# Optimization experiments

Measured on AMD Instinct MI355X. Metric: run time of the kernel, lower is better.

## Reference

```python
import jax, jax.numpy as jnp
import numpy as np

D_MODEL = 768
N_HEADS = 12
D_HEAD = 64
WINDOW = 32
LOOK_BACK = 1
PAD_VALUE = 0
IGNORE = -1000000.0
BS = 2
SEQ = 1024  # multiple of WINDOW so autopad is a no-op


def setup_inputs() -> dict:
    key = jax.random.key(0)
    k0, k1, k2, k3, k4 = jax.random.split(key, 5)
    x = jax.random.normal(k0, (BS, SEQ, D_MODEL), dtype=jnp.float32)
    W_abcde = jax.random.normal(k1, (D_MODEL, 5 * N_HEADS * D_HEAD), dtype=jnp.float32) * (1.0 / np.sqrt(D_MODEL))
    b_abcde = jax.random.normal(k2, (5 * N_HEADS * D_HEAD,), dtype=jnp.float32) * 0.02
    W_O = jax.random.normal(k3, (N_HEADS * D_HEAD, D_MODEL), dtype=jnp.float32) * (1.0 / np.sqrt(N_HEADS * D_HEAD))
    b_O = jax.random.normal(k4, (D_MODEL,), dtype=jnp.float32) * 0.02
    return dict(x=x, W_abcde=W_abcde, b_abcde=b_abcde, W_O=W_O, b_O=b_O)


def _look_around(t, backward=LOOK_BACK, pad_value=0):
    # t: (B, n_windows, window, ...). Pad along the windows axis, then
    # concatenate [prev_window, current_window] along the within-window axis.
    nw = t.shape[1]
    pad = [(0, 0)] * t.ndim
    pad[1] = (backward, 0)
    tp = jnp.pad(t, pad, constant_values=pad_value)
    return jnp.concatenate([tp[:, i:i + nw] for i in range(backward + 1)], axis=2)


def reference(x, W_abcde, b_abcde, W_O, b_O):
    bs, ts, _ = x.shape
    nw = ts // WINDOW
    B = bs * N_HEADS

    abcde = x @ W_abcde + b_abcde                       # (bs, ts, 5*h*d)
    abcde = abcde.reshape(bs, ts, 5, N_HEADS, D_HEAD)
    abcde = jnp.transpose(abcde, (2, 0, 3, 1, 4))       # (5, bs, h, ts, d)
    abcde = abcde.reshape(5, B, nw, WINDOW, D_HEAD)     # windowed
    a, b, c, d, e = abcde[0], abcde[1], abcde[2], abcde[3], abcde[4]

    # position ids per window, and their look-around version (pad_value = cfg.pad_value)
    seq = jnp.arange(ts, dtype=jnp.int32).reshape(1, nw, WINDOW)      # (1, nw, w)
    bb_t = _look_around(seq, LOOK_BACK, PAD_VALUE)                    # (1, nw, 2w)
    qi = seq[..., :, None, None]    # query position  (n axis)
    kj = bb_t[..., None, :, None]   # a-token position (m axis)
    lk = bb_t[..., None, None, :]   # b-token position (l axis)
    # masked unless: t_b <= t_query AND t_a < t_b
    mask = (qi < lk) | (lk <= kj)   # (1, nw, w, 2w, 2w)

    la_a = _look_around(a)
    la_b = _look_around(b)
    la_d = _look_around(d)
    la_e = _look_around(e)

    # triple-interaction scores: (B, nw, w, 2w, 2w)
    attn = jnp.einsum('xnid,xnjd,xnkd->xnijk', c, la_a, la_b)
    # mask causal-invalid entries, and (as in original) exact zeros (padding dots)
    attn = jnp.where(mask | (attn == 0.0), IGNORE, attn)
    attn = attn / D_HEAD
    shp = attn.shape
    score = jax.nn.softmax(attn.reshape(shp[0], shp[1], shp[2], -1), axis=-1).reshape(shp)

    # dual value combine: D at the a-position (m), E at the b-position (l)
    z = jnp.einsum('xnijk,xnjd->xnid', score, la_d) \
        + jnp.einsum('xnijk,xnkd->xnid', score, la_e)

    z = z.reshape(bs, N_HEADS, nw, WINDOW, D_HEAD)
    z = jnp.transpose(z, (0, 2, 3, 1, 4)).reshape(bs, ts, N_HEADS * D_HEAD)
    return z @ W_O + b_O
```

## Files before the change

kernel.cpp:

```cpp
#include <hip/hip_runtime.h>
#include <math.h>
#include <stdint.h>

#define NH     12
#define DH     64
#define WIN    32
#define SEQL   1024
#define BSZ    2
#define NW     (SEQL / WIN)
#define DMODEL 768
#define NCOL   (5 * NH * DH)

typedef __attribute__((ext_vector_type(4))) float f32x4;
typedef __attribute__((ext_vector_type(8))) short bf16x8;
typedef unsigned short u16;

static __device__ __forceinline__ u16 f2bf(float f) {
  union { float f; unsigned u; } v; v.f = f;
  unsigned r = v.u + 0x7fffu + ((v.u >> 16) & 1u);
  return (u16)(r >> 16);
}
static __device__ __forceinline__ float bf2f(u16 u) {
  union { unsigned u; float f; } v; v.u = ((unsigned)u) << 16;
  return v.f;
}

typedef const __attribute__((address_space(1))) unsigned int* as1_cu32;
typedef __attribute__((address_space(3))) unsigned int* as3_u32;
static __device__ __forceinline__ void gload_lds16(const void* g, void* l) {
  __builtin_amdgcn_global_load_lds(
      reinterpret_cast<as1_cu32>(reinterpret_cast<uintptr_t>(g)),
      reinterpret_cast<as3_u32>(reinterpret_cast<uintptr_t>(l)), 16, 0, 0);
}

__global__ __launch_bounds__(256)
void cvt_bf16_kernel(const float* __restrict__ S, u16* __restrict__ D, int n4) {
  const int i = blockIdx.x * 256 + threadIdx.x;
  if (i < n4) {
    const float4 v = reinterpret_cast<const float4*>(S)[i];
    ushort4 o;
    o.x = f2bf(v.x); o.y = f2bf(v.y); o.z = f2bf(v.z); o.w = f2bf(v.w);
    reinterpret_cast<ushort4*>(D)[i] = o;
  }
}

__global__ __launch_bounds__(256)
void transpose_cvt_kernel(const float* __restrict__ S, u16* __restrict__ D,
                          int K, int N) {
  __shared__ u16 tile[64][68];
  const int tid = threadIdx.x;
  const int n0 = blockIdx.x * 64;
  const int k0 = blockIdx.y * 64;
#pragma unroll
  for (int pass = 0; pass < 4; ++pass) {
    const int r = pass * 16 + (tid >> 4);
    const int c = (tid & 15) << 2;
    const float4 v = *reinterpret_cast<const float4*>(&S[(size_t)(k0 + r) * N + n0 + c]);
    tile[c + 0][r] = f2bf(v.x); tile[c + 1][r] = f2bf(v.y);
    tile[c + 2][r] = f2bf(v.z); tile[c + 3][r] = f2bf(v.w);
  }
  __syncthreads();
#pragma unroll
  for (int pass = 0; pass < 4; ++pass) {
    const int rn = pass * 16 + (tid >> 4);
    const int ck = (tid & 15) << 2;
    ushort4 o;
    o.x = tile[rn][ck + 0]; o.y = tile[rn][ck + 1];
    o.z = tile[rn][ck + 2]; o.w = tile[rn][ck + 3];
    *reinterpret_cast<ushort4*>(&D[(size_t)(n0 + rn) * K + k0 + ck]) = o;
  }
}

template<int BM, int BN, int WAVES_M, int WAVES_N, bool OUT_BF16>
__global__ __launch_bounds__(256)
void gemm_mfma_kernel(const u16* __restrict__ A, const u16* __restrict__ Bt,
                      const float* __restrict__ bias, void* __restrict__ Cout,
                      int M, int N, int K) {
  constexpr int BK = 64;
  constexpr int MT = BM / (16 * WAVES_M);
  constexpr int NT = BN / (16 * WAVES_N);
  constexpr int CHA = BM / 8;
  constexpr int CHB = BN / 8;
  __shared__ __align__(16) u16 As[BM * BK];
  __shared__ __align__(16) u16 Bs[BN * BK];

  const int tid  = threadIdx.x;
  const int w    = tid >> 6;
  const int lane = tid & 63;
  const int m16  = lane & 15;
  const int g    = lane >> 4;
  const int wr   = w / WAVES_N;
  const int wc   = w % WAVES_N;
  const int bm   = blockIdx.y * BM;
  const int bn   = blockIdx.x * BN;

  const int srow   = lane >> 3;
  const int srcCol = ((lane & 7) ^ srow) << 3;

  f32x4 acc[MT][NT];
#pragma unroll
  for (int i = 0; i < MT; ++i)
#pragma unroll
    for (int j = 0; j < NT; ++j) {
      f32x4 z = {0.f, 0.f, 0.f, 0.f};
      acc[i][j] = z;
    }

  for (int k0 = 0; k0 < K; k0 += BK) {
#pragma unroll
    for (int c = 0; c < CHA / 4; ++c) {
      const int ch = w * (CHA / 4) + c;
      const int r  = ch * 8 + srow;
      gload_lds16(A + (size_t)(bm + r) * K + k0 + srcCol, As + ch * 512);
    }
#pragma unroll
    for (int c = 0; c < CHB / 4; ++c) {
      const int ch = w * (CHB / 4) + c;
      const int r  = ch * 8 + srow;
      gload_lds16(Bt + (size_t)(bn + r) * K + k0 + srcCol, Bs + ch * 512);
    }
    __syncthreads();

#pragma unroll
    for (int kk = 0; kk < 2; ++kk) {
      const int cs = (((kk << 2) + g) ^ (m16 & 7)) << 3;
      bf16x8 af[MT], bf[NT];
#pragma unroll
      for (int i = 0; i < MT; ++i) {
        const int r = wr * (16 * MT) + i * 16 + m16;
        af[i] = *reinterpret_cast<const bf16x8*>(&As[r * 64 + cs]);
      }
#pragma unroll
      for (int j = 0; j < NT; ++j) {
        const int r = wc * (16 * NT) + j * 16 + m16;
        bf[j] = *reinterpret_cast<const bf16x8*>(&Bs[r * 64 + cs]);
      }
#pragma unroll
      for (int i = 0; i < MT; ++i)
#pragma unroll
        for (int j = 0; j < NT; ++j)
          acc[i][j] = __builtin_amdgcn_mfma_f32_16x16x32_bf16(af[i], bf[j], acc[i][j], 0, 0, 0);
    }
    __syncthreads();
  }

#pragma unroll
  for (int i = 0; i < MT; ++i) {
#pragma unroll
    for (int j = 0; j < NT; ++j) {
      const int col = bn + wc * 16 * NT + j * 16 + m16;
      const float bcol = bias[col];
#pragma unroll
      for (int rr = 0; rr < 4; ++rr) {
        const int row = bm + wr * 16 * MT + i * 16 + g * 4 + rr;
        const float v = acc[i][j][rr] + bcol;
        if (OUT_BF16)
          reinterpret_cast<u16*>(Cout)[(size_t)row * N + col] = f2bf(v);
        else
          reinterpret_cast<float*>(Cout)[(size_t)row * N + col] = v;
      }
    }
  }
}

__global__ __launch_bounds__(512, 3)
void attn_mfma_kernel(const u16* __restrict__ Y, u16* __restrict__ Z) {
  __shared__ __align__(16) u16 DET[64][136];
  __shared__ __align__(16) u16 RQ[32][136];
  __shared__ float tot_lds[32];

  const int n  = blockIdx.x;
  const int bh = blockIdx.y;
  const int bi = bh / NH;
  const int h  = bh % NH;
  const int tid  = threadIdx.x;
  const int wv   = tid >> 6;
  const int lane = tid & 63;
  const int m16  = lane & 15;
  const int g    = lane >> 4;
  const u16* Yb = Y + (size_t)bi * SEQL * NCOL;

  {
    const int j  = lane;
    const int r8 = wv * 8;
    const int t  = n * WIN - WIN + j;
    if (t >= 0) {
      const bf16x8 dv = *reinterpret_cast<const bf16x8*>(
          Yb + (size_t)t * NCOL + (3 * NH + h) * DH + r8);
      const bf16x8 ev = *reinterpret_cast<const bf16x8*>(
          Yb + (size_t)t * NCOL + (4 * NH + h) * DH + r8);
#pragma unroll
      for (int e = 0; e < 8; ++e) {
        DET[r8 + e][j]      = (u16)dv[e];
        DET[r8 + e][64 + j] = (u16)ev[e];
      }
    } else {
#pragma unroll
      for (int e = 0; e < 8; ++e) {
        DET[r8 + e][j] = 0;
        DET[r8 + e][64 + j] = 0;
      }
    }
  }

  bf16x8 afr[4][2], bfrb[4][2];
#pragma unroll
  for (int jt = 0; jt < 4; ++jt) {
    const int t = n * WIN - WIN + jt * 16 + m16;
#pragma unroll
    for (int ks = 0; ks < 2; ++ks) {
      if (n == 0 && jt < 2) {
        bf16x8 z = {0, 0, 0, 0, 0, 0, 0, 0};
        afr[jt][ks] = z;
        bfrb[jt][ks] = z;
      } else {
        afr[jt][ks] = *reinterpret_cast<const bf16x8*>(
            Yb + (size_t)t * NCOL + h * DH + ks * 32 + g * 8);
        bfrb[jt][ks] = *reinterpret_cast<const bf16x8*>(
            Yb + (size_t)t * NCOL + (NH + h) * DH + ks * 32 + g * 8);
      }
    }
  }

  const float K2 = 0.015625f * 1.44269504088896341f;
  const u16* crow_base = Yb + (size_t)(n * WIN) * NCOL + (2 * NH + h) * DH;

  for (int ii = 0; ii < 4; ++ii) {
    const int i = wv * 4 + ii;
    const u16* cp = crow_base + (size_t)i * NCOL;

    bf16x8 craw[2];
    craw[0] = *reinterpret_cast<const bf16x8*>(cp + g * 8);
    craw[1] = *reinterpret_cast<const bf16x8*>(cp + 32 + g * 8);
    float cf[2][8];
#pragma unroll
    for (int ks = 0; ks < 2; ++ks)
#pragma unroll
      for (int e = 0; e < 8; ++e) cf[ks][e] = bf2f((u16)craw[ks][e]);

    f32x4 acc[4][4];
#pragma unroll
    for (int jt = 0; jt < 4; ++jt)
#pragma unroll
      for (int kt = 0; kt < 4; ++kt) {
        f32x4 z = {0.f, 0.f, 0.f, 0.f};
        acc[jt][kt] = z;
      }

#pragma unroll
    for (int ks = 0; ks < 2; ++ks) {
#pragma unroll
      for (int kt = 0; kt < 4; ++kt) {
        bf16x8 vf;
#pragma unroll
        for (int e = 0; e < 8; ++e)
          vf[e] = (short)f2bf(bf2f((u16)bfrb[kt][ks][e]) * cf[ks][e]);
#pragma unroll
        for (int jt = 0; jt < 4; ++jt)
          acc[jt][kt] = __builtin_amdgcn_mfma_f32_16x16x32_bf16(afr[jt][ks], vf, acc[jt][kt], 0, 0, 0);
      }
    }

    float rp[16], qp[4];
#pragma unroll
    for (int u = 0; u < 16; ++u) rp[u] = 0.f;
#pragma unroll
    for (int u = 0; u < 4; ++u) qp[u] = 0.f;
#pragma unroll
    for (int kt = 0; kt < 4; ++kt) {
      const int k = kt * 16 + m16;
      const bool ck = k <= i + 32;
#pragma unroll
      for (int jt = 0; jt < 4; ++jt) {
        const bool rok = (n > 0) || (jt >= 2);
#pragma unroll
        for (int r = 0; r < 4; ++r) {
          const int j = jt * 16 + g * 4 + r;
          const bool valid = ck && rok && (k > j);
          const float e = valid ? exp2f(acc[jt][kt][r] * K2) : 0.f;
          rp[jt * 4 + r] += e;
          qp[kt] += e;
        }
      }
    }

    float rsel, qsel, tp;
    if (n == 0 && i == 0) {
      rsel = 1.f; qsel = 1.f; tp = 64.f;
    } else {
      float tin = (qp[0] + qp[1]) + (qp[2] + qp[3]);
#pragma unroll
      for (int off = 1; off <= 32; off <<= 1) tin += __shfl_xor(tin, off);
      tp = tin;

      float v8[8];
      {
        const bool b = (m16 & 1) != 0;
#pragma unroll
        for (int t2 = 0; t2 < 8; ++t2) {
          const float keep = b ? rp[2 * t2 + 1] : rp[2 * t2];
          const float send = b ? rp[2 * t2] : rp[2 * t2 + 1];
          v8[t2] = keep + __shfl_xor(send, 1);
        }
      }
      float v4s[4];
      {
        const bool b = (m16 & 2) != 0;
#pragma unroll
        for (int t2 = 0; t2 < 4; ++t2) {
          const float keep = b ? v8[2 * t2 + 1] : v8[2 * t2];
          const float send = b ? v8[2 * t2] : v8[2 * t2 + 1];
          v4s[t2] = keep + __shfl_xor(send, 2);
        }
      }
      float v2s[2];
      {
        const bool b = (m16 & 4) != 0;
#pragma unroll
        for (int t2 = 0; t2 < 2; ++t2) {
          const float keep = b ? v4s[2 * t2 + 1] : v4s[2 * t2];
          const float send = b ? v4s[2 * t2] : v4s[2 * t2 + 1];
          v2s[t2] = keep + __shfl_xor(send, 4);
        }
      }
      {
        const bool b = (m16 & 8) != 0;
        const float keep = b ? v2s[1] : v2s[0];
        const float send = b ? v2s[0] : v2s[1];
        rsel = keep + __shfl_xor(send, 8);
      }
      float q2[2];
      {
        const bool b = (g & 1) != 0;
#pragma unroll
        for (int t2 = 0; t2 < 2; ++t2) {
          const float keep = b ? qp[2 * t2 + 1] : qp[2 * t2];
          const float send = b ? qp[2 * t2] : qp[2 * t2 + 1];
          q2[t2] = keep + __shfl_xor(send, 16);
        }
      }
      {
        const bool b = (g & 2) != 0;
        const float keep = b ? q2[1] : q2[0];
        const float send = b ? q2[0] : q2[1];
        qsel = keep + __shfl_xor(send, 32);
      }
    }

    RQ[i][(m16 >> 2) * 16 + g * 4 + (m16 & 3)] = f2bf(rsel);
    RQ[i][64 + g * 16 + m16] = f2bf(qsel);
    if (lane == 0) tot_lds[i] = tp;
  }

  __syncthreads();

  const int mt = wv >> 2;
  const int nt = wv & 3;
  f32x4 zac = {0.f, 0.f, 0.f, 0.f};
#pragma unroll
  for (int kq = 0; kq < 4; ++kq) {
    const bf16x8 bf = *reinterpret_cast<const bf16x8*>(&DET[nt * 16 + m16][kq * 32 + g * 8]);
    const bf16x8 af = *reinterpret_cast<const bf16x8*>(&RQ[mt * 16 + m16][kq * 32 + g * 8]);
    zac = __builtin_amdgcn_mfma_f32_16x16x32_bf16(af, bf, zac, 0, 0, 0);
  }
#pragma unroll
  for (int r = 0; r < 4; ++r) {
    const int i = mt * 16 + g * 4 + r;
    const int d = nt * 16 + m16;
    Z[((size_t)bi * SEQL + n * WIN + i) * (NH * DH) + h * DH + d] =
        f2bf(zac[r] / tot_lds[i]);
  }
}

extern "C" void kernel_launch(void* const* d_in, const int* in_sizes, int n_in,
                              void* d_out, int out_size, void* d_ws, size_t ws_size,
                              hipStream_t stream) {
  const float* x        = (const float*)d_in[0];
  const float* W_abcde  = (const float*)d_in[1];
  const float* b_abcde  = (const float*)d_in[2];
  const float* W_O      = (const float*)d_in[3];
  const float* b_O      = (const float*)d_in[4];
  float* out = (float*)d_out;

  const int M = BSZ * SEQL;

  u16* Yb  = (u16*)d_ws;
  u16* xb  = Yb  + (size_t)M * NCOL;
  u16* Wt  = xb  + (size_t)M * DMODEL;
  u16* WOt = Wt  + (size_t)NCOL * DMODEL;
  u16* Zb  = WOt + (size_t)(NH * DH) * DMODEL;

  cvt_bf16_kernel<<<(M * DMODEL / 4 + 255) / 256, 256, 0, stream>>>(x, xb, M * DMODEL / 4);
  transpose_cvt_kernel<<<dim3(NCOL / 64, DMODEL / 64), 256, 0, stream>>>(W_abcde, Wt, DMODEL, NCOL);
  transpose_cvt_kernel<<<dim3((NH * DH) / 64, DMODEL / 64), 256, 0, stream>>>(W_O, WOt, DMODEL, NH * DH);

  gemm_mfma_kernel<128, 128, 2, 2, true><<<dim3(NCOL / 128, M / 128), 256, 0, stream>>>(
      xb, Wt, b_abcde, Yb, M, NCOL, DMODEL);

  attn_mfma_kernel<<<dim3(NW, BSZ * NH), 512, 0, stream>>>(Yb, Zb);

  gemm_mfma_kernel<64, 64, 2, 2, false><<<dim3((NH * DH) / 64, M / 64), 256, 0, stream>>>(
      Zb, WOt, b_O, out, M, DMODEL, NH * DH);
}
```

Baseline: 161.7 us.

## Merge prep kernels and skip masked MFMA tiles in windowed triple attention

The three conversion/transpose kernels become a single prep launch that dispatches on block index, which removes two launches. In the attention kernel, the scale K2 is folded into the c vector, and MFMA tiles where every entry is masked (jt > kt) are skipped. The masking logic is simplified, and exp2f, the packed bf16 conversion and the division are replaced by hardware intrinsics (exp2, v_cvt_pk_bf16_f32, rcp). Risks are small precision differences from the fast rcp/exp and the changed rounding of the packed conversion.

After: 146.2 us. 1.11x faster.

```diff
diff --git a/kernel.cpp b/kernel.cpp
--- a/kernel.cpp
+++ b/kernel.cpp
@@ -24,6 +24,11 @@
   union { unsigned u; float f; } v; v.u = ((unsigned)u) << 16;
   return v.f;
 }
+static __device__ __forceinline__ unsigned cvt_pk_bf16(float lo, float hi) {
+  unsigned p;
+  asm("v_cvt_pk_bf16_f32 %0, %1, %2" : "=v"(p) : "v"(lo), "v"(hi));
+  return p;
+}
 
 typedef const __attribute__((address_space(1))) unsigned int* as1_cu32;
 typedef __attribute__((address_space(3))) unsigned int* as3_u32;
@@ -34,23 +39,32 @@
 }
 
 __global__ __launch_bounds__(256)
-void cvt_bf16_kernel(const float* __restrict__ S, u16* __restrict__ D, int n4) {
-  const int i = blockIdx.x * 256 + threadIdx.x;
-  if (i < n4) {
-    const float4 v = reinterpret_cast<const float4*>(S)[i];
+void prep_kernel(const float* __restrict__ x, const float* __restrict__ W,
+                 const float* __restrict__ WO, u16* __restrict__ xb,
+                 u16* __restrict__ Wt, u16* __restrict__ WOt) {
+  __shared__ u16 tile[64][68];
+  const int bid = blockIdx.x;
+  const int tid = threadIdx.x;
+
+  if (bid < 1536) {
+    const int i = bid * 256 + tid;
+    const float4 v = reinterpret_cast<const float4*>(x)[i];
     ushort4 o;
     o.x = f2bf(v.x); o.y = f2bf(v.y); o.z = f2bf(v.z); o.w = f2bf(v.w);
-    reinterpret_cast<ushort4*>(D)[i] = o;
-  }
-}
-
-__global__ __launch_bounds__(256)
-void transpose_cvt_kernel(const float* __restrict__ S, u16* __restrict__ D,
-                          int K, int N) {
-  __shared__ u16 tile[64][68];
-  const int tid = threadIdx.x;
-  const int n0 = blockIdx.x * 64;
-  const int k0 = blockIdx.y * 64;
+    reinterpret_cast<ushort4*>(xb)[i] = o;
+    return;
+  }
+
+  const float* S; u16* D; int K, N, n0, k0;
+  if (bid < 2256) {
+    const int b = bid - 1536;
+    S = W; D = Wt; K = DMODEL; N = NCOL;
+    n0 = (b % 60) * 64; k0 = (b / 60) * 64;
+  } else {
+    const int b = bid - 2256;
+    S = WO; D = WOt; K = DMODEL; N = NH * DH;
+    n0 = (b % 12) * 64; k0 = (b / 12) * 64;
+  }
 #pragma unroll
   for (int pass = 0; pass < 4; ++pass) {
     const int r = pass * 16 + (tid >> 4);
@@ -178,6 +192,7 @@
   const int lane = tid & 63;
   const int m16  = lane & 15;
   const int g    = lane >> 4;
+  const int g4   = g << 2;
   const u16* Yb = Y + (size_t)bi * SEQL * NCOL;
 
   {
@@ -236,13 +251,13 @@
 #pragma unroll
     for (int ks = 0; ks < 2; ++ks)
 #pragma unroll
-      for (int e = 0; e < 8; ++e) cf[ks][e] = bf2f((u16)craw[ks][e]);
+      for (int e = 0; e < 8; ++e) cf[ks][e] = bf2f((u16)craw[ks][e]) * K2;
 
     f32x4 acc[4][4];
 #pragma unroll
-    for (int jt = 0; jt < 4; ++jt)
-#pragma unroll
-      for (int kt = 0; kt < 4; ++kt) {
+    for (int kt = 0; kt < 4; ++kt)
+#pragma unroll
+      for (int jt = 0; jt <= kt; ++jt) {
         f32x4 z = {0.f, 0.f, 0.f, 0.f};
         acc[jt][kt] = z;
       }
@@ -253,10 +268,13 @@
       for (int kt = 0; kt < 4; ++kt) {
         bf16x8 vf;
 #pragma unroll
-        for (int e = 0; e < 8; ++e)
-          vf[e] = (short)f2bf(bf2f((u16)bfrb[kt][ks][e]) * cf[ks][e]);
-#pragma unroll
-        for (int jt = 0; jt < 4; ++jt)
+        for (int e = 0; e < 8; e += 2) {
+          const float lo = bf2f((u16)bfrb[kt][ks][e])     * cf[ks][e];
+          const float hi = bf2f((u16)bfrb[kt][ks][e + 1]) * cf[ks][e + 1];
+          reinterpret_cast<unsigned*>(&vf)[e >> 1] = cvt_pk_bf16(lo, hi);
+        }
+#pragma unroll
+        for (int jt = 0; jt <= kt; ++jt)
           acc[jt][kt] = __builtin_amdgcn_mfma_f32_16x16x32_bf16(afr[jt][ks], vf, acc[jt][kt], 0, 0, 0);
       }
     }
@@ -268,16 +286,15 @@
     for (int u = 0; u < 4; ++u) qp[u] = 0.f;
 #pragma unroll
     for (int kt = 0; kt < 4; ++kt) {
-      const int k = kt * 16 + m16;
-      const bool ck = k <= i + 32;
-#pragma unroll
-      for (int jt = 0; jt < 4; ++jt) {
-        const bool rok = (n > 0) || (jt >= 2);
+      const bool ck = (kt < 2) ? true : (kt * 16 + m16 <= i + 32);
+#pragma unroll
+      for (int jt = 0; jt <= kt; ++jt) {
+        const bool rok = (jt >= 2) || (n > 0);
+        const bool base = ck && rok;
 #pragma unroll
         for (int r = 0; r < 4; ++r) {
-          const int j = jt * 16 + g * 4 + r;
-          const bool valid = ck && rok && (k > j);
-          const float e = valid ? exp2f(acc[jt][kt][r] * K2) : 0.f;
+          const bool valid = (jt == kt) ? (base && (m16 > g4 + r)) : base;
+          const float e = valid ? __builtin_amdgcn_exp2f(acc[jt][kt][r]) : 0.f;
           rp[jt * 4 + r] += e;
           qp[kt] += e;
         }
@@ -347,7 +364,7 @@
       }
     }
 
-    RQ[i][(m16 >> 2) * 16 + g * 4 + (m16 & 3)] = f2bf(rsel);
+    RQ[i][(m16 >> 2) * 16 + g4 + (m16 & 3)] = f2bf(rsel);
     RQ[i][64 + g * 16 + m16] = f2bf(qsel);
     if (lane == 0) tot_lds[i] = tp;
   }
@@ -365,10 +382,11 @@
   }
 #pragma unroll
   for (int r = 0; r < 4; ++r) {
-    const int i = mt * 16 + g * 4 + r;
+    const int i = mt * 16 + g4 + r;
     const int d = nt * 16 + m16;
+    const float inv = __builtin_amdgcn_rcpf(tot_lds[i]);
     Z[((size_t)bi * SEQL + n * WIN + i) * (NH * DH) + h * DH + d] =
-        f2bf(zac[r] / tot_lds[i]);
+        f2bf(zac[r] * inv);
   }
 }
 
@@ -390,9 +408,7 @@
   u16* WOt = Wt  + (size_t)NCOL * DMODEL;
   u16* Zb  = WOt + (size_t)(NH * DH) * DMODEL;
 
-  cvt_bf16_kernel<<<(M * DMODEL / 4 + 255) / 256, 256, 0, stream>>>(x, xb, M * DMODEL / 4);
-  transpose_cvt_kernel<<<dim3(NCOL / 64, DMODEL / 64), 256, 0, stream>>>(W_abcde, Wt, DMODEL, NCOL);
-  transpose_cvt_kernel<<<dim3((NH * DH) / 64, DMODEL / 64), 256, 0, stream>>>(W_O, WOt, DMODEL, NH * DH);
+  prep_kernel<<<2400, 256, 0, stream>>>(x, W_abcde, W_O, xb, Wt, WOt);
 
   gemm_mfma_kernel<128, 128, 2, 2, true><<<dim3(NCOL / 128, M / 128), 256, 0, stream>>>(
       xb, Wt, b_abcde, Yb, M, NCOL, DMODEL);
```
